# Kernel optimization log

Measured on AMD Instinct MI355X. Metric: run time of the kernel, lower is better.

Reference implementation:

```python
import jax, jax.numpy as jnp
import numpy as np

B, D, H, W = 8, 1024, 64, 64
NH = 16
HD = D // NH
EPS = 1e-5


def _pos_encoding(n, d, dtype):
    # standard 1D sinusoidal PE over flattened spatial positions, shape (n, d)
    pos = jnp.arange(n, dtype=jnp.float32)[:, None]
    i = jnp.arange(d)[None, :]
    rates = 1.0 / (10000.0 ** ((2 * (i // 2)).astype(jnp.float32) / d))
    ang = pos * rates
    pe = jnp.where(i % 2 == 0, jnp.sin(ang), jnp.cos(ang))
    return pe.astype(dtype)


def setup_inputs() -> dict:
    key = jax.random.key(0)
    ks = jax.random.split(key, 4)
    x = jax.random.normal(ks[0], (B, D, H, W), dtype=jnp.float32)
    context_token = jax.random.normal(ks[1], (B, 1, D), dtype=jnp.float32)
    Wqkv = jax.random.normal(ks[2], (3 * D, D), dtype=jnp.float32) * 0.02
    bqkv = jnp.zeros((3 * D,), dtype=jnp.float32)
    Wo = jax.random.normal(ks[3], (D, D), dtype=jnp.float32) * 0.02
    bo = jnp.zeros((D,), dtype=jnp.float32)
    gamma = jnp.ones((D,), dtype=jnp.float32)
    beta = jnp.zeros((D,), dtype=jnp.float32)
    return {"x": x, "context_token": context_token, "Wqkv": Wqkv, "bqkv": bqkv,
            "Wo": Wo, "bo": bo, "gamma": gamma, "beta": beta}


def reference(x, context_token, Wqkv, bqkv, Wo, bo, gamma, beta):
    b, d, h, w = x.shape
    hw = h * w
    # x_flat: (B, HW, D); add positional encoding
    x_flat = x.reshape(b, d, hw).transpose(0, 2, 1)
    x_flat = x_flat + _pos_encoding(hw, d, x.dtype)[None]
    xc = jnp.concatenate([context_token, x_flat], axis=1)  # (B, S, D), S = HW+1
    s = hw + 1

    qkv = xc @ Wqkv.T + bqkv                                 # (B, S, 3D)
    q, k, v = jnp.split(qkv, 3, axis=-1)
    k = k.reshape(b, s, NH, HD)
    v = v.reshape(b, s, NH, HD)
    scale = 1.0 / jnp.sqrt(jnp.asarray(HD, x.dtype))

    # Star attention: CLS query (row 0) attends to all keys
    q0 = q[:, 0].reshape(b, NH, HD)                          # (B, NH, HD)
    scores = jnp.einsum('bhd,bshd->bhs', q0, k) * scale      # (B, NH, S)
    probs = jax.nn.softmax(scores, axis=-1)
    cls_out = jnp.einsum('bhs,bshd->bhd', probs, v).reshape(b, d)

    # Token queries attend only to the CLS key -> softmax over 1 elem = 1 -> v_cls
    v_cls = v[:, 0].reshape(b, d)                            # (B, D)
    tok_out = jnp.broadcast_to(v_cls[:, None, :], (b, hw, d))

    attn = jnp.concatenate([cls_out[:, None, :], tok_out], axis=1)  # (B, S, D)
    attn = attn @ Wo.T + bo

    res = attn + xc
    mu = jnp.mean(res, axis=-1, keepdims=True)
    var = jnp.mean((res - mu) ** 2, axis=-1, keepdims=True)
    y = (res - mu) * jax.lax.rsqrt(var + EPS) * gamma + beta

    context_token_out = y[:, 0:1, :]
    feature_map_out = y[:, 1:, :].transpose(0, 2, 1).reshape(b, d, h, w)
    return feature_map_out, context_token_out
```

## Files before the change

kernel.cpp:

```cpp
#include <hip/hip_runtime.h>
#include <math.h>

#define B_ 8
#define D_ 1024
#define HW_ 4096
#define NH_ 16
#define EPS_ 1e-5f

#define PE_OFF   0u
#define UT_OFF   4194304u
#define TB_OFF   4325376u
#define SC_OFF   4333568u
#define Q0_OFF   4857856u
#define VCLS_OFF 4866048u
#define P0_OFF   4874240u
#define MU_OFF   4874368u
#define RS_OFF   4907136u
#define W_OFF    4939904u
#define CLS_OFF  5070976u
#define R0_OFF   5079168u

__global__ void k_pe(float* __restrict__ pe) {
    int idx = blockIdx.x * 256 + threadIdx.x;
    int p  = idx & (HW_ - 1);
    int dp = idx >> 12;
    float e = (float)(2 * dp);
    float rate = exp2f(e * (-13.287712379549449f / 1024.0f));
    float ang = (float)p * rate;
    float s, c;
    sincosf(ang, &s, &c);
    pe[(size_t)(2 * dp) * HW_ + p]     = s;
    pe[(size_t)(2 * dp + 1) * HW_ + p] = c;
}

__global__ void k_qv(const float* __restrict__ Wqkv, const float* __restrict__ bqkv,
                     const float* __restrict__ ctx,
                     float* __restrict__ q0, float* __restrict__ vcls) {
    int wid  = (blockIdx.x * 256 + threadIdx.x) >> 6;
    int lane = threadIdx.x & 63;
    int isv  = wid >> 13;
    int r    = wid & 8191;
    int b = r >> 10, i = r & 1023;
    int row = isv ? (2 * D_ + i) : i;
    const float4* wr = (const float4*)(Wqkv + (size_t)row * D_);
    const float4* cb = (const float4*)(ctx + b * D_);
    float acc = 0.0f;
    for (int k = lane; k < 256; k += 64) {
        float4 a = wr[k], c = cb[k];
        acc += a.x * c.x + a.y * c.y + a.z * c.z + a.w * c.w;
    }
    for (int o = 32; o; o >>= 1) acc += __shfl_down(acc, o);
    if (lane == 0) {
        float v = acc + bqkv[row];
        if (isv) vcls[b * D_ + i] = v; else q0[b * D_ + i] = v;
    }
}

__global__ void k_u_tb(const float* __restrict__ Wqkv,
                       const float* __restrict__ Wo, const float* __restrict__ bo,
                       const float* __restrict__ q0, const float* __restrict__ vcls,
                       float* __restrict__ u_t, float* __restrict__ t_b) {
    if (blockIdx.x < 128) {
        int b = blockIdx.x >> 4, h = blockIdx.x & 15;
        int t = threadIdx.x;
        float a0 = 0, a1 = 0, a2 = 0, a3 = 0;
        const float* q0h = q0 + b * D_ + h * 64;
        for (int j = 0; j < 64; ++j) {
            float qj = q0h[j];
            const float* wr = Wqkv + (size_t)(D_ + h * 64 + j) * D_;
            a0 += qj * wr[t];
            a1 += qj * wr[t + 256];
            a2 += qj * wr[t + 512];
            a3 += qj * wr[t + 768];
        }
        float* ub = u_t + (size_t)(b * D_) * NH_ + h;
        ub[(size_t)t * 16]          = 0.125f * a0;
        ub[(size_t)(t + 256) * 16]  = 0.125f * a1;
        ub[(size_t)(t + 512) * 16]  = 0.125f * a2;
        ub[(size_t)(t + 768) * 16]  = 0.125f * a3;
    } else {
        int wid  = (blockIdx.x - 128) * 4 + (threadIdx.x >> 6);
        int lane = threadIdx.x & 63;
        int b = wid >> 10, i = wid & 1023;
        const float4* wr = (const float4*)(Wo + (size_t)i * D_);
        const float4* vb = (const float4*)(vcls + b * D_);
        float acc = 0.0f;
        for (int k = lane; k < 256; k += 64) {
            float4 a = wr[k], c = vb[k];
            acc += a.x * c.x + a.y * c.y + a.z * c.z + a.w * c.w;
        }
        for (int o = 32; o; o >>= 1) acc += __shfl_down(acc, o);
        if (lane == 0) t_b[b * D_ + i] = acc + bo[i];
    }
}

__global__ __launch_bounds__(1024) void k_scores(
        const float* __restrict__ x, const float* __restrict__ pe,
        const float* __restrict__ u_t, const float* __restrict__ t_b,
        float* __restrict__ scores, float* __restrict__ mu_o, float* __restrict__ rs_o) {
    int tid = threadIdx.x;
    int wave = tid >> 6, lane = tid & 63;
    int b = blockIdx.y;
    int pbase = blockIdx.x * 128;
    int p0 = pbase + lane * 2;
    const float* xb  = x  + (size_t)b * D_ * HW_ + p0;
    const float* peb = pe + p0;
    const float* tb  = t_b + b * D_;
    float acc0[16], acc1[16];
    #pragma unroll
    for (int h = 0; h < 16; ++h) { acc0[h] = 0.f; acc1[h] = 0.f; }
    float s0 = 0.f, s1 = 0.f, q0s = 0.f, q1s = 0.f;
    int dbeg = wave * 64;
    #pragma unroll 2
    for (int i = 0; i < 64; ++i) {
        int d = dbeg + i;
        float2 xv = *(const float2*)(xb  + (size_t)d * HW_);
        float2 pv = *(const float2*)(peb + (size_t)d * HW_);
        float xc0 = xv.x + pv.x, xc1 = xv.y + pv.y;
        float tbd = tb[d];
        float r0 = xc0 + tbd, r1 = xc1 + tbd;
        s0 += r0; s1 += r1; q0s += r0 * r0; q1s += r1 * r1;
        const float* up = u_t + ((size_t)(b * D_ + d) << 4);
        #pragma unroll
        for (int h = 0; h < 16; ++h) {
            float u = up[h];
            acc0[h] += u * xc0;
            acc1[h] += u * xc1;
        }
    }
    __shared__ float red[16][4][128];
    #pragma unroll 1
    for (int c = 0; c < 4; ++c) {
        #pragma unroll
        for (int j = 0; j < 4; ++j) {
            red[wave][j][lane * 2]     = acc0[4 * c + j];
            red[wave][j][lane * 2 + 1] = acc1[4 * c + j];
        }
        __syncthreads();
        if (tid < 512) {
            int hh = tid >> 7, p = tid & 127;
            float s = 0.f;
            #pragma unroll
            for (int w2 = 0; w2 < 16; ++w2) s += red[w2][hh][p];
            scores[(size_t)(b * 16 + 4 * c + hh) * HW_ + pbase + p] = s;
        }
        __syncthreads();
    }
    red[wave][0][lane * 2]     = s0;
    red[wave][0][lane * 2 + 1] = s1;
    red[wave][1][lane * 2]     = q0s;
    red[wave][1][lane * 2 + 1] = q1s;
    __syncthreads();
    if (tid < 128) {
        float S = 0.f, Q = 0.f;
        #pragma unroll
        for (int w2 = 0; w2 < 16; ++w2) { S += red[w2][0][tid]; Q += red[w2][1][tid]; }
        float mu = S * (1.0f / 1024.0f);
        float var = Q * (1.0f / 1024.0f) - mu * mu;
        mu_o[b * HW_ + pbase + tid] = mu;
        rs_o[b * HW_ + pbase + tid] = rsqrtf(var + EPS_);
    }
}

__global__ void k_softmax(const float* __restrict__ scores, const float* __restrict__ u_t,
                          const float* __restrict__ ctx,
                          float* __restrict__ probs_tok, float* __restrict__ probs0) {
    int b = blockIdx.x >> 4, h = blockIdx.x & 15;
    int t = threadIdx.x;
    __shared__ float lds[256];
    float part = 0.0f;
    for (int d = t; d < D_; d += 256)
        part += u_t[(size_t)(b * D_ + d) * 16 + h] * ctx[b * D_ + d];
    lds[t] = part; __syncthreads();
    for (int o = 128; o; o >>= 1) { if (t < o) lds[t] += lds[t + o]; __syncthreads(); }
    float s0 = lds[0];
    __syncthreads();
    const float4* sr = (const float4*)(scores + (size_t)(b * 16 + h) * HW_);
    float4 v[4];
    float m = s0;
    #pragma unroll
    for (int k = 0; k < 4; ++k) {
        v[k] = sr[t + 256 * k];
        m = fmaxf(m, fmaxf(fmaxf(v[k].x, v[k].y), fmaxf(v[k].z, v[k].w)));
    }
    lds[t] = m; __syncthreads();
    for (int o = 128; o; o >>= 1) { if (t < o) lds[t] = fmaxf(lds[t], lds[t + o]); __syncthreads(); }
    m = lds[0];
    __syncthreads();
    float zs = 0.0f;
    #pragma unroll
    for (int k = 0; k < 4; ++k) {
        v[k].x = expf(v[k].x - m); v[k].y = expf(v[k].y - m);
        v[k].z = expf(v[k].z - m); v[k].w = expf(v[k].w - m);
        zs += v[k].x + v[k].y + v[k].z + v[k].w;
    }
    float e0 = expf(s0 - m);
    lds[t] = zs; __syncthreads();
    for (int o = 128; o; o >>= 1) { if (t < o) lds[t] += lds[t + o]; __syncthreads(); }
    float inv = 1.0f / (lds[0] + e0);
    float4* pr = (float4*)(probs_tok + (size_t)(b * 16 + h) * HW_);
    #pragma unroll
    for (int k = 0; k < 4; ++k) {
        float4 o4 = v[k];
        o4.x *= inv; o4.y *= inv; o4.z *= inv; o4.w *= inv;
        pr[t + 256 * k] = o4;
    }
    if (t == 0) probs0[b * 16 + h] = e0 * inv;
}

__global__ __launch_bounds__(256) void k_wacc2(
        const float* __restrict__ x, const float* __restrict__ pe,
        const float* __restrict__ probs, const float* __restrict__ p0v,
        const float* __restrict__ ctx, const float* __restrict__ t_b,
        const float* __restrict__ mu_i, const float* __restrict__ rs_i,
        const float* __restrict__ gamma, const float* __restrict__ beta,
        float* __restrict__ w, float* __restrict__ out) {
    int wave = threadIdx.x >> 6, lane = threadIdx.x & 63;
    int b = blockIdx.y;
    int d0 = (blockIdx.x * 4 + wave) * 4;
    const float* xb = x + (size_t)b * D_ * HW_;
    const float* pb = probs + (size_t)b * 16 * HW_;
    float* ob = out + (size_t)b * D_ * HW_;
    float tbv[4], gv[4], bev[4];
    #pragma unroll
    for (int r = 0; r < 4; ++r) {
        tbv[r] = t_b[b * D_ + d0 + r];
        gv[r]  = gamma[d0 + r];
        bev[r] = beta[d0 + r];
    }
    float acc[4][16];
    #pragma unroll
    for (int r = 0; r < 4; ++r)
        #pragma unroll
        for (int h = 0; h < 16; ++h) acc[r][h] = 0.f;
    #pragma unroll 1
    for (int it = 0; it < 16; ++it) {
        int p = it * 256 + lane * 4;
        float4 xc4[4];
        #pragma unroll
        for (int r = 0; r < 4; ++r) {
            float4 xv = *(const float4*)(xb + (size_t)(d0 + r) * HW_ + p);
            float4 pv = *(const float4*)(pe + (size_t)(d0 + r) * HW_ + p);
            xc4[r].x = xv.x + pv.x; xc4[r].y = xv.y + pv.y;
            xc4[r].z = xv.z + pv.z; xc4[r].w = xv.w + pv.w;
        }
        float4 m4 = *(const float4*)(mu_i + b * HW_ + p);
        float4 r4 = *(const float4*)(rs_i + b * HW_ + p);
        #pragma unroll
        for (int r = 0; r < 4; ++r) {
            float4 o4;
            o4.x = (xc4[r].x + tbv[r] - m4.x) * r4.x * gv[r] + bev[r];
            o4.y = (xc4[r].y + tbv[r] - m4.y) * r4.y * gv[r] + bev[r];
            o4.z = (xc4[r].z + tbv[r] - m4.z) * r4.z * gv[r] + bev[r];
            o4.w = (xc4[r].w + tbv[r] - m4.w) * r4.w * gv[r] + bev[r];
            *(float4*)(ob + (size_t)(d0 + r) * HW_ + p) = o4;
        }
        #pragma unroll
        for (int h = 0; h < 16; ++h) {
            float4 pr = *(const float4*)(pb + (size_t)h * HW_ + p);
            #pragma unroll
            for (int r = 0; r < 4; ++r)
                acc[r][h] += pr.x * xc4[r].x + pr.y * xc4[r].y +
                             pr.z * xc4[r].z + pr.w * xc4[r].w;
        }
    }
    #pragma unroll
    for (int r = 0; r < 4; ++r)
        #pragma unroll
        for (int h = 0; h < 16; ++h) {
            float v = acc[r][h];
            for (int o = 32; o; o >>= 1) v += __shfl_down(v, o);
            acc[r][h] = v;
        }
    if (lane == 0) {
        #pragma unroll
        for (int h = 0; h < 16; ++h) {
            float pp = p0v[b * 16 + h];
            #pragma unroll
            for (int r = 0; r < 4; ++r)
                w[(size_t)(b * 16 + h) * D_ + d0 + r] = acc[r][h] + pp * ctx[b * D_ + d0 + r];
        }
    }
}

__global__ void k_cls(const float* __restrict__ Wqkv, const float* __restrict__ bqkv,
                      const float* __restrict__ w, float* __restrict__ cls) {
    int wid  = (blockIdx.x * 256 + threadIdx.x) >> 6;
    int lane = threadIdx.x & 63;
    int b = wid >> 10, i = wid & 1023, h = i >> 6;
    const float4* wr = (const float4*)(Wqkv + (size_t)(2 * D_ + i) * D_);
    const float4* wb = (const float4*)(w + (size_t)(b * 16 + h) * D_);
    float acc = 0.0f;
    for (int k = lane; k < 256; k += 64) {
        float4 a = wr[k], c = wb[k];
        acc += a.x * c.x + a.y * c.y + a.z * c.z + a.w * c.w;
    }
    for (int o = 32; o; o >>= 1) acc += __shfl_down(acc, o);
    if (lane == 0) cls[b * D_ + i] = acc + bqkv[2 * D_ + i];
}

__global__ void k_attn0(const float* __restrict__ Wo, const float* __restrict__ bo,
                        const float* __restrict__ cls, const float* __restrict__ ctx,
                        float* __restrict__ res0) {
    int wid  = (blockIdx.x * 256 + threadIdx.x) >> 6;
    int lane = threadIdx.x & 63;
    int b = wid >> 10, i = wid & 1023;
    const float4* wr = (const float4*)(Wo + (size_t)i * D_);
    const float4* cb = (const float4*)(cls + b * D_);
    float acc = 0.0f;
    for (int k = lane; k < 256; k += 64) {
        float4 a = wr[k], c = cb[k];
        acc += a.x * c.x + a.y * c.y + a.z * c.z + a.w * c.w;
    }
    for (int o = 32; o; o >>= 1) acc += __shfl_down(acc, o);
    if (lane == 0) res0[b * D_ + i] = acc + bo[i] + ctx[b * D_ + i];
}

__global__ void k_ln0(const float* __restrict__ res0, const float* __restrict__ gamma,
                      const float* __restrict__ beta, float* __restrict__ out) {
    int b = blockIdx.x, t = threadIdx.x;
    __shared__ float lds[512];
    float v[4];
    float s = 0.0f, sq = 0.0f;
    #pragma unroll
    for (int k = 0; k < 4; ++k) {
        v[k] = res0[b * D_ + t + 256 * k];
        s += v[k]; sq += v[k] * v[k];
    }
    lds[t] = s; lds[256 + t] = sq; __syncthreads();
    for (int o = 128; o; o >>= 1) {
        if (t < o) { lds[t] += lds[t + o]; lds[256 + t] += lds[256 + t + o]; }
        __syncthreads();
    }
    float mu = lds[0] * (1.0f / D_);
    float var = lds[256] * (1.0f / D_) - mu * mu;
    float rstd = rsqrtf(var + EPS_);
    #pragma unroll
    for (int k = 0; k < 4; ++k) {
        int i = t + 256 * k;
        out[(size_t)B_ * D_ * HW_ + b * D_ + i] = (v[k] - mu) * rstd * gamma[i] + beta[i];
    }
}

extern "C" void kernel_launch(void* const* d_in, const int* in_sizes, int n_in,
                              void* d_out, int out_size, void* d_ws, size_t ws_size,
                              hipStream_t stream) {
    const float* x     = (const float*)d_in[0];
    const float* ctx   = (const float*)d_in[1];
    const float* Wqkv  = (const float*)d_in[2];
    const float* bqkv  = (const float*)d_in[3];
    const float* Wo    = (const float*)d_in[4];
    const float* bo    = (const float*)d_in[5];
    const float* gamma = (const float*)d_in[6];
    const float* beta  = (const float*)d_in[7];
    float* out = (float*)d_out;
    float* ws  = (float*)d_ws;

    float* pe   = ws + PE_OFF;
    float* u_t  = ws + UT_OFF;
    float* t_b  = ws + TB_OFF;
    float* sc   = ws + SC_OFF;
    float* q0   = ws + Q0_OFF;
    float* vcls = ws + VCLS_OFF;
    float* p0   = ws + P0_OFF;
    float* mu   = ws + MU_OFF;
    float* rs   = ws + RS_OFF;
    float* w    = ws + W_OFF;
    float* cls  = ws + CLS_OFF;
    float* r0   = ws + R0_OFF;

    k_pe<<<dim3(8192), dim3(256), 0, stream>>>(pe);
    k_qv<<<dim3(4096), dim3(256), 0, stream>>>(Wqkv, bqkv, ctx, q0, vcls);
    k_u_tb<<<dim3(2176), dim3(256), 0, stream>>>(Wqkv, Wo, bo, q0, vcls, u_t, t_b);
    k_scores<<<dim3(32, 8), dim3(1024), 0, stream>>>(x, pe, u_t, t_b, sc, mu, rs);
    k_softmax<<<dim3(128), dim3(256), 0, stream>>>(sc, u_t, ctx, sc, p0);
    k_wacc2<<<dim3(64, 8), dim3(256), 0, stream>>>(x, pe, sc, p0, ctx, t_b, mu, rs,
                                                   gamma, beta, w, out);
    k_cls<<<dim3(2048), dim3(256), 0, stream>>>(Wqkv, bqkv, w, cls);
    k_attn0<<<dim3(2048), dim3(256), 0, stream>>>(Wo, bo, cls, ctx, r0);
    k_ln0<<<dim3(8), dim3(256), 0, stream>>>(r0, gamma, beta, out);
}
```

Measured before the change: 429.0 us.

## Split scores over D and weighted accumulation over positions into partial buffers

The scores kernel now splits the 1024-wide D reduction into 8 slices. Each slice writes partial scores and partial sum and sum-of-squares to workspace. A new stats kernel and the softmax kernel sum those partials. The weighted-accumulation kernel splits positions into 4 chunks, writing partial w vectors that the cls kernel sums. The aim is many more, smaller blocks (float4 loads, 256 threads) so the GPU fills better than with one 1024-thread block per CU, at the cost of extra partial-buffer traffic and one more launch.

```diff
diff --git a/kernel.cpp b/kernel.cpp
--- a/kernel.cpp
+++ b/kernel.cpp
@@ -10,15 +10,17 @@
 #define PE_OFF   0u
 #define UT_OFF   4194304u
 #define TB_OFF   4325376u
-#define SC_OFF   4333568u
-#define Q0_OFF   4857856u
-#define VCLS_OFF 4866048u
-#define P0_OFF   4874240u
-#define MU_OFF   4874368u
-#define RS_OFF   4907136u
-#define W_OFF    4939904u
-#define CLS_OFF  5070976u
-#define R0_OFF   5079168u
+#define SCP_OFF  4333568u
+#define SP_OFF   8527872u
+#define QP_OFF   8790016u
+#define WP_OFF   8527872u
+#define Q0_OFF   9052160u
+#define VCLS_OFF 9060352u
+#define P0_OFF   9068544u
+#define MU_OFF   9068672u
+#define RS_OFF   9101440u
+#define CLS_OFF  9134208u
+#define R0_OFF   9142400u
 
 __global__ void k_pe(float* __restrict__ pe) {
     int idx = blockIdx.x * 256 + threadIdx.x;
@@ -94,77 +96,83 @@
     }
 }
 
-__global__ __launch_bounds__(1024) void k_scores(
+#define FMA4(A, U) { (A).x += (U) * xc.x; (A).y += (U) * xc.y; \
+                     (A).z += (U) * xc.z; (A).w += (U) * xc.w; }
+
+__global__ __launch_bounds__(256, 4) void k_scores2(
         const float* __restrict__ x, const float* __restrict__ pe,
         const float* __restrict__ u_t, const float* __restrict__ t_b,
-        float* __restrict__ scores, float* __restrict__ mu_o, float* __restrict__ rs_o) {
+        float* __restrict__ scp, float* __restrict__ sp, float* __restrict__ qp) {
     int tid = threadIdx.x;
     int wave = tid >> 6, lane = tid & 63;
     int b = blockIdx.y;
-    int pbase = blockIdx.x * 128;
-    int p0 = pbase + lane * 2;
+    int ptile = (blockIdx.x & 15) * 256;
+    int ds = blockIdx.x >> 4;
+    int p0 = ptile + lane * 4;
+    int dbeg = ds * 128 + wave * 32;
     const float* xb  = x  + (size_t)b * D_ * HW_ + p0;
     const float* peb = pe + p0;
     const float* tb  = t_b + b * D_;
-    float acc0[16], acc1[16];
-    #pragma unroll
-    for (int h = 0; h < 16; ++h) { acc0[h] = 0.f; acc1[h] = 0.f; }
-    float s0 = 0.f, s1 = 0.f, q0s = 0.f, q1s = 0.f;
-    int dbeg = wave * 64;
-    #pragma unroll 2
-    for (int i = 0; i < 64; ++i) {
+    float4 acc[16];
+    #pragma unroll
+    for (int h = 0; h < 16; ++h) acc[h] = make_float4(0.f, 0.f, 0.f, 0.f);
+    float4 s4 = make_float4(0.f, 0.f, 0.f, 0.f);
+    float4 q4 = make_float4(0.f, 0.f, 0.f, 0.f);
+    #pragma unroll 4
+    for (int i = 0; i < 32; ++i) {
         int d = dbeg + i;
-        float2 xv = *(const float2*)(xb  + (size_t)d * HW_);
-        float2 pv = *(const float2*)(peb + (size_t)d * HW_);
-        float xc0 = xv.x + pv.x, xc1 = xv.y + pv.y;
+        float4 xv = *(const float4*)(xb  + (size_t)d * HW_);
+        float4 pv = *(const float4*)(peb + (size_t)d * HW_);
+        float4 xc = make_float4(xv.x + pv.x, xv.y + pv.y, xv.z + pv.z, xv.w + pv.w);
         float tbd = tb[d];
-        float r0 = xc0 + tbd, r1 = xc1 + tbd;
-        s0 += r0; s1 += r1; q0s += r0 * r0; q1s += r1 * r1;
-        const float* up = u_t + ((size_t)(b * D_ + d) << 4);
-        #pragma unroll
-        for (int h = 0; h < 16; ++h) {
-            float u = up[h];
-            acc0[h] += u * xc0;
-            acc1[h] += u * xc1;
-        }
-    }
-    __shared__ float red[16][4][128];
+        float4 r = make_float4(xc.x + tbd, xc.y + tbd, xc.z + tbd, xc.w + tbd);
+        s4.x += r.x; s4.y += r.y; s4.z += r.z; s4.w += r.w;
+        q4.x += r.x * r.x; q4.y += r.y * r.y; q4.z += r.z * r.z; q4.w += r.w * r.w;
+        const float4* up = (const float4*)(u_t + ((size_t)(b * D_ + d) << 4));
+        float4 u0 = up[0], u1 = up[1], u2 = up[2], u3 = up[3];
+        FMA4(acc[0],  u0.x) FMA4(acc[1],  u0.y) FMA4(acc[2],  u0.z) FMA4(acc[3],  u0.w)
+        FMA4(acc[4],  u1.x) FMA4(acc[5],  u1.y) FMA4(acc[6],  u1.z) FMA4(acc[7],  u1.w)
+        FMA4(acc[8],  u2.x) FMA4(acc[9],  u2.y) FMA4(acc[10], u2.z) FMA4(acc[11], u2.w)
+        FMA4(acc[12], u3.x) FMA4(acc[13], u3.y) FMA4(acc[14], u3.z) FMA4(acc[15], u3.w)
+    }
+    __shared__ float red[4][4][256];
     #pragma unroll 1
     for (int c = 0; c < 4; ++c) {
+        if (c) __syncthreads();
+        #pragma unroll
+        for (int j = 0; j < 4; ++j)
+            *(float4*)&red[wave][j][lane * 4] = acc[c * 4 + j];
+        __syncthreads();
         #pragma unroll
         for (int j = 0; j < 4; ++j) {
-            red[wave][j][lane * 2]     = acc0[4 * c + j];
-            red[wave][j][lane * 2 + 1] = acc1[4 * c + j];
-        }
-        __syncthreads();
-        if (tid < 512) {
-            int hh = tid >> 7, p = tid & 127;
-            float s = 0.f;
-            #pragma unroll
-            for (int w2 = 0; w2 < 16; ++w2) s += red[w2][hh][p];
-            scores[(size_t)(b * 16 + 4 * c + hh) * HW_ + pbase + p] = s;
-        }
-        __syncthreads();
-    }
-    red[wave][0][lane * 2]     = s0;
-    red[wave][0][lane * 2 + 1] = s1;
-    red[wave][1][lane * 2]     = q0s;
-    red[wave][1][lane * 2 + 1] = q1s;
+            float s = red[0][j][tid] + red[1][j][tid] + red[2][j][tid] + red[3][j][tid];
+            scp[(size_t)ds * 524288 + (size_t)(b * 16 + c * 4 + j) * HW_ + ptile + tid] = s;
+        }
+    }
     __syncthreads();
-    if (tid < 128) {
-        float S = 0.f, Q = 0.f;
-        #pragma unroll
-        for (int w2 = 0; w2 < 16; ++w2) { S += red[w2][0][tid]; Q += red[w2][1][tid]; }
-        float mu = S * (1.0f / 1024.0f);
-        float var = Q * (1.0f / 1024.0f) - mu * mu;
-        mu_o[b * HW_ + pbase + tid] = mu;
-        rs_o[b * HW_ + pbase + tid] = rsqrtf(var + EPS_);
-    }
-}
-
-__global__ void k_softmax(const float* __restrict__ scores, const float* __restrict__ u_t,
-                          const float* __restrict__ ctx,
-                          float* __restrict__ probs_tok, float* __restrict__ probs0) {
+    *(float4*)&red[wave][0][lane * 4] = s4;
+    *(float4*)&red[wave][1][lane * 4] = q4;
+    __syncthreads();
+    float S = red[0][0][tid] + red[1][0][tid] + red[2][0][tid] + red[3][0][tid];
+    float Q = red[0][1][tid] + red[1][1][tid] + red[2][1][tid] + red[3][1][tid];
+    sp[ds * 32768 + b * HW_ + ptile + tid] = S;
+    qp[ds * 32768 + b * HW_ + ptile + tid] = Q;
+}
+
+__global__ void k_stats(const float* __restrict__ sp, const float* __restrict__ qp,
+                        float* __restrict__ mu_o, float* __restrict__ rs_o) {
+    int i = blockIdx.x * 256 + threadIdx.x;
+    float S = 0.f, Q = 0.f;
+    #pragma unroll
+    for (int ds = 0; ds < 8; ++ds) { S += sp[ds * 32768 + i]; Q += qp[ds * 32768 + i]; }
+    float mu = S * (1.0f / 1024.0f);
+    float var = Q * (1.0f / 1024.0f) - mu * mu;
+    mu_o[i] = mu;
+    rs_o[i] = rsqrtf(var + EPS_);
+}
+
+__global__ void k_softmax2(float* __restrict__ scp, const float* __restrict__ u_t,
+                           const float* __restrict__ ctx, float* __restrict__ probs0) {
     int b = blockIdx.x >> 4, h = blockIdx.x & 15;
     int t = threadIdx.x;
     __shared__ float lds[256];
@@ -175,13 +183,19 @@
     for (int o = 128; o; o >>= 1) { if (t < o) lds[t] += lds[t + o]; __syncthreads(); }
     float s0 = lds[0];
     __syncthreads();
-    const float4* sr = (const float4*)(scores + (size_t)(b * 16 + h) * HW_);
+    size_t row = (size_t)(b * 16 + h) * HW_;
     float4 v[4];
     float m = s0;
     #pragma unroll
     for (int k = 0; k < 4; ++k) {
-        v[k] = sr[t + 256 * k];
-        m = fmaxf(m, fmaxf(fmaxf(v[k].x, v[k].y), fmaxf(v[k].z, v[k].w)));
+        float4 vk = make_float4(0.f, 0.f, 0.f, 0.f);
+        #pragma unroll
+        for (int ds = 0; ds < 8; ++ds) {
+            float4 pvk = ((const float4*)(scp + (size_t)ds * 524288 + row))[t + 256 * k];
+            vk.x += pvk.x; vk.y += pvk.y; vk.z += pvk.z; vk.w += pvk.w;
+        }
+        v[k] = vk;
+        m = fmaxf(m, fmaxf(fmaxf(vk.x, vk.y), fmaxf(vk.z, vk.w)));
     }
     lds[t] = m; __syncthreads();
     for (int o = 128; o; o >>= 1) { if (t < o) lds[t] = fmaxf(lds[t], lds[t + o]); __syncthreads(); }
@@ -198,7 +212,7 @@
     lds[t] = zs; __syncthreads();
     for (int o = 128; o; o >>= 1) { if (t < o) lds[t] += lds[t + o]; __syncthreads(); }
     float inv = 1.0f / (lds[0] + e0);
-    float4* pr = (float4*)(probs_tok + (size_t)(b * 16 + h) * HW_);
+    float4* pr = (float4*)(scp + row);
     #pragma unroll
     for (int k = 0; k < 4; ++k) {
         float4 o4 = v[k];
@@ -208,16 +222,18 @@
     if (t == 0) probs0[b * 16 + h] = e0 * inv;
 }
 
-__global__ __launch_bounds__(256) void k_wacc2(
+__global__ __launch_bounds__(256, 4) void k_wacc3(
         const float* __restrict__ x, const float* __restrict__ pe,
         const float* __restrict__ probs, const float* __restrict__ p0v,
         const float* __restrict__ ctx, const float* __restrict__ t_b,
         const float* __restrict__ mu_i, const float* __restrict__ rs_i,
         const float* __restrict__ gamma, const float* __restrict__ beta,
-        float* __restrict__ w, float* __restrict__ out) {
+        float* __restrict__ wp, float* __restrict__ out) {
     int wave = threadIdx.x >> 6, lane = threadIdx.x & 63;
     int b = blockIdx.y;
-    int d0 = (blockIdx.x * 4 + wave) * 4;
+    int dgrp = blockIdx.x >> 2, pc = blockIdx.x & 3;
+    int d0 = (dgrp * 4 + wave) * 4;
+    int pbase = pc * 1024;
     const float* xb = x + (size_t)b * D_ * HW_;
     const float* pb = probs + (size_t)b * 16 * HW_;
     float* ob = out + (size_t)b * D_ * HW_;
@@ -234,8 +250,8 @@
         #pragma unroll
         for (int h = 0; h < 16; ++h) acc[r][h] = 0.f;
     #pragma unroll 1
-    for (int it = 0; it < 16; ++it) {
-        int p = it * 256 + lane * 4;
+    for (int it = 0; it < 4; ++it) {
+        int p = pbase + it * 256 + lane * 4;
         float4 xc4[4];
         #pragma unroll
         for (int r = 0; r < 4; ++r) {
@@ -275,25 +291,31 @@
     if (lane == 0) {
         #pragma unroll
         for (int h = 0; h < 16; ++h) {
-            float pp = p0v[b * 16 + h];
+            float extra = (pc == 0) ? p0v[b * 16 + h] : 0.f;
             #pragma unroll
             for (int r = 0; r < 4; ++r)
-                w[(size_t)(b * 16 + h) * D_ + d0 + r] = acc[r][h] + pp * ctx[b * D_ + d0 + r];
-        }
-    }
-}
-
-__global__ void k_cls(const float* __restrict__ Wqkv, const float* __restrict__ bqkv,
-                      const float* __restrict__ w, float* __restrict__ cls) {
+                wp[(size_t)pc * 131072 + (size_t)(b * 16 + h) * D_ + d0 + r] =
+                    acc[r][h] + extra * ctx[b * D_ + d0 + r];
+        }
+    }
+}
+
+__global__ void k_cls2(const float* __restrict__ Wqkv, const float* __restrict__ bqkv,
+                       const float* __restrict__ wp, float* __restrict__ cls) {
     int wid  = (blockIdx.x * 256 + threadIdx.x) >> 6;
     int lane = threadIdx.x & 63;
     int b = wid >> 10, i = wid & 1023, h = i >> 6;
     const float4* wr = (const float4*)(Wqkv + (size_t)(2 * D_ + i) * D_);
-    const float4* wb = (const float4*)(w + (size_t)(b * 16 + h) * D_);
+    const float4* w0 = (const float4*)(wp + (size_t)(b * 16 + h) * D_);
     float acc = 0.0f;
     for (int k = lane; k < 256; k += 64) {
-        float4 a = wr[k], c = wb[k];
-        acc += a.x * c.x + a.y * c.y + a.z * c.z + a.w * c.w;
+        float4 a = wr[k];
+        float4 c0 = w0[k], c1 = w0[k + 32768], c2 = w0[k + 65536], c3 = w0[k + 98304];
+        float cx = c0.x + c1.x + c2.x + c3.x;
+        float cy = c0.y + c1.y + c2.y + c3.y;
+        float cz = c0.z + c1.z + c2.z + c3.z;
+        float cw = c0.w + c1.w + c2.w + c3.w;
+        acc += a.x * cx + a.y * cy + a.z * cz + a.w * cw;
     }
     for (int o = 32; o; o >>= 1) acc += __shfl_down(acc, o);
     if (lane == 0) cls[b * D_ + i] = acc + bqkv[2 * D_ + i];
@@ -359,24 +381,27 @@
     float* pe   = ws + PE_OFF;
     float* u_t  = ws + UT_OFF;
     float* t_b  = ws + TB_OFF;
-    float* sc   = ws + SC_OFF;
+    float* scp  = ws + SCP_OFF;
+    float* sp   = ws + SP_OFF;
+    float* qp   = ws + QP_OFF;
+    float* wpb  = ws + WP_OFF;
     float* q0   = ws + Q0_OFF;
     float* vcls = ws + VCLS_OFF;
     float* p0   = ws + P0_OFF;
     float* mu   = ws + MU_OFF;
     float* rs   = ws + RS_OFF;
-    float* w    = ws + W_OFF;
     float* cls  = ws + CLS_OFF;
     float* r0   = ws + R0_OFF;
 
     k_pe<<<dim3(8192), dim3(256), 0, stream>>>(pe);
     k_qv<<<dim3(4096), dim3(256), 0, stream>>>(Wqkv, bqkv, ctx, q0, vcls);
     k_u_tb<<<dim3(2176), dim3(256), 0, stream>>>(Wqkv, Wo, bo, q0, vcls, u_t, t_b);
-    k_scores<<<dim3(32, 8), dim3(1024), 0, stream>>>(x, pe, u_t, t_b, sc, mu, rs);
-    k_softmax<<<dim3(128), dim3(256), 0, stream>>>(sc, u_t, ctx, sc, p0);
-    k_wacc2<<<dim3(64, 8), dim3(256), 0, stream>>>(x, pe, sc, p0, ctx, t_b, mu, rs,
-                                                   gamma, beta, w, out);
-    k_cls<<<dim3(2048), dim3(256), 0, stream>>>(Wqkv, bqkv, w, cls);
+    k_scores2<<<dim3(128, 8), dim3(256), 0, stream>>>(x, pe, u_t, t_b, scp, sp, qp);
+    k_softmax2<<<dim3(128), dim3(256), 0, stream>>>(scp, u_t, ctx, p0);
+    k_stats<<<dim3(128), dim3(256), 0, stream>>>(sp, qp, mu, rs);
+    k_wacc3<<<dim3(256, 8), dim3(256), 0, stream>>>(x, pe, scp, p0, ctx, t_b, mu, rs,
+                                                    gamma, beta, wpb, out);
+    k_cls2<<<dim3(2048), dim3(256), 0, stream>>>(Wqkv, bqkv, wpb, cls);
     k_attn0<<<dim3(2048), dim3(256), 0, stream>>>(Wo, bo, cls, ctx, r0);
     k_ln0<<<dim3(8), dim3(256), 0, stream>>>(r0, gamma, beta, out);
 }
```

Result: slower. 727.7 us (+69.6%).

## Compute positional encoding inline and split score reduction over D for parallelism

Applied to the files above, without the earlier changes.

Drops the precomputed positional-encoding buffer and recomputes sin/cos on the fly with hardware sin/cos intrinsics, removing a large 16 MB write plus two re-reads of it. The scores kernel is split across 8 D-slices (2048 blocks of 256 threads instead of 256 blocks of 1024) with u_t staged in LDS. It writes partial scores and partial stats, which a new stats kernel and the softmax then reduce. Probabilities are stored transposed (position-major, 16 heads contiguous) and the weighted-accumulate kernel uses one d row per wave for more blocks. The cost is extra partial-sum traffic, an extra launch, and possible precision loss from the approximate hardware sin/cos on large angles.

```diff
diff --git a/kernel.cpp b/kernel.cpp
--- a/kernel.cpp
+++ b/kernel.cpp
@@ -7,31 +7,23 @@
 #define NH_ 16
 #define EPS_ 1e-5f
 
-#define PE_OFF   0u
-#define UT_OFF   4194304u
-#define TB_OFF   4325376u
-#define SC_OFF   4333568u
-#define Q0_OFF   4857856u
-#define VCLS_OFF 4866048u
-#define P0_OFF   4874240u
-#define MU_OFF   4874368u
-#define RS_OFF   4907136u
-#define W_OFF    4939904u
-#define CLS_OFF  5070976u
-#define R0_OFF   5079168u
-
-__global__ void k_pe(float* __restrict__ pe) {
-    int idx = blockIdx.x * 256 + threadIdx.x;
-    int p  = idx & (HW_ - 1);
-    int dp = idx >> 12;
-    float e = (float)(2 * dp);
-    float rate = exp2f(e * (-13.287712379549449f / 1024.0f));
-    float ang = (float)p * rate;
-    float s, c;
-    sincosf(ang, &s, &c);
-    pe[(size_t)(2 * dp) * HW_ + p]     = s;
-    pe[(size_t)(2 * dp + 1) * HW_ + p] = c;
-}
+#define RATE_C (-13.287712379549449f / 512.0f)
+#define INV2PI 0.15915494309189535f
+
+#define UT_OFF   0u
+#define TB_OFF   131072u
+#define SCP_OFF  139264u
+#define SP_OFF   4333568u
+#define QP_OFF   4595712u
+#define PT_OFF   4857856u
+#define W_OFF    5382144u
+#define Q0_OFF   5513216u
+#define VCLS_OFF 5521408u
+#define P0_OFF   5529600u
+#define MU_OFF   5529728u
+#define RS_OFF   5562496u
+#define CLS_OFF  5595264u
+#define R0_OFF   5603456u
 
 __global__ void k_qv(const float* __restrict__ Wqkv, const float* __restrict__ bqkv,
                      const float* __restrict__ ctx,
@@ -94,77 +86,121 @@
     }
 }
 
-__global__ __launch_bounds__(1024) void k_scores(
-        const float* __restrict__ x, const float* __restrict__ pe,
-        const float* __restrict__ u_t, const float* __restrict__ t_b,
-        float* __restrict__ scores, float* __restrict__ mu_o, float* __restrict__ rs_o) {
+__global__ __launch_bounds__(256) void k_scoresA(
+        const float* __restrict__ x, const float* __restrict__ u_t,
+        const float* __restrict__ t_b,
+        float* __restrict__ scp, float* __restrict__ sp, float* __restrict__ qp) {
     int tid = threadIdx.x;
     int wave = tid >> 6, lane = tid & 63;
     int b = blockIdx.y;
-    int pbase = blockIdx.x * 128;
-    int p0 = pbase + lane * 2;
-    const float* xb  = x  + (size_t)b * D_ * HW_ + p0;
-    const float* peb = pe + p0;
-    const float* tb  = t_b + b * D_;
-    float acc0[16], acc1[16];
-    #pragma unroll
-    for (int h = 0; h < 16; ++h) { acc0[h] = 0.f; acc1[h] = 0.f; }
-    float s0 = 0.f, s1 = 0.f, q0s = 0.f, q1s = 0.f;
-    int dbeg = wave * 64;
+    int ptile = (blockIdx.x & 31) * 128;
+    int ds = blockIdx.x >> 5;
+    int p0 = ptile + lane * 2;
+
+    __shared__ float uts[128 * 16];
+    __shared__ float tbs[128];
+    __shared__ float rrev[64];
+    __shared__ float red[4][4][128];
+    {
+        const float4* src = (const float4*)(u_t + ((size_t)(b * D_ + ds * 128) << 4));
+        float4* dst = (float4*)uts;
+        dst[tid]       = src[tid];
+        dst[tid + 256] = src[tid + 256];
+        if (tid < 128) tbs[tid] = t_b[b * D_ + ds * 128 + tid];
+        if (tid < 64)  rrev[tid] = exp2f((float)(ds * 64 + tid) * RATE_C) * INV2PI;
+    }
+    __syncthreads();
+
+    float accA[16], accB[16];
+    #pragma unroll
+    for (int h = 0; h < 16; ++h) { accA[h] = 0.f; accB[h] = 0.f; }
+    float sA = 0.f, sB = 0.f, qA = 0.f, qB = 0.f;
+    const float* xb = x + (size_t)b * D_ * HW_ + (size_t)(ds * 128 + wave * 32) * HW_ + p0;
+    float fp0 = (float)p0, fp1 = fp0 + 1.0f;
+
     #pragma unroll 2
-    for (int i = 0; i < 64; ++i) {
-        int d = dbeg + i;
-        float2 xv = *(const float2*)(xb  + (size_t)d * HW_);
-        float2 pv = *(const float2*)(peb + (size_t)d * HW_);
-        float xc0 = xv.x + pv.x, xc1 = xv.y + pv.y;
-        float tbd = tb[d];
-        float r0 = xc0 + tbd, r1 = xc1 + tbd;
-        s0 += r0; s1 += r1; q0s += r0 * r0; q1s += r1 * r1;
-        const float* up = u_t + ((size_t)(b * D_ + d) << 4);
-        #pragma unroll
-        for (int h = 0; h < 16; ++h) {
-            float u = up[h];
-            acc0[h] += u * xc0;
-            acc1[h] += u * xc1;
-        }
-    }
-    __shared__ float red[16][4][128];
+    for (int i = 0; i < 16; ++i) {
+        int dloc = wave * 32 + i * 2;
+        float2 xe = *(const float2*)(xb + (size_t)(i * 2) * HW_);
+        float2 xo = *(const float2*)(xb + (size_t)(i * 2 + 1) * HW_);
+        float rr = rrev[wave * 16 + i];
+        float rv0 = fp0 * rr, rv1 = fp1 * rr;
+        rv0 -= floorf(rv0); rv1 -= floorf(rv1);
+        float sn0 = __builtin_amdgcn_sinf(rv0), cs0 = __builtin_amdgcn_cosf(rv0);
+        float sn1 = __builtin_amdgcn_sinf(rv1), cs1 = __builtin_amdgcn_cosf(rv1);
+        float xAe = xe.x + sn0, xBe = xe.y + sn1;
+        float xAo = xo.x + cs0, xBo = xo.y + cs1;
+        float te = tbs[dloc], to = tbs[dloc + 1];
+        float rAe = xAe + te, rBe = xBe + te, rAo = xAo + to, rBo = xBo + to;
+        sA += rAe + rAo; sB += rBe + rBo;
+        qA += rAe * rAe + rAo * rAo; qB += rBe * rBe + rBo * rBo;
+        const float4* u4 = (const float4*)(uts + dloc * 16);
+        float4 e0 = u4[0], e1 = u4[1], o0 = u4[4], o1 = u4[5];
+        accA[0] += e0.x * xAe + o0.x * xAo;  accB[0] += e0.x * xBe + o0.x * xBo;
+        accA[1] += e0.y * xAe + o0.y * xAo;  accB[1] += e0.y * xBe + o0.y * xBo;
+        accA[2] += e0.z * xAe + o0.z * xAo;  accB[2] += e0.z * xBe + o0.z * xBo;
+        accA[3] += e0.w * xAe + o0.w * xAo;  accB[3] += e0.w * xBe + o0.w * xBo;
+        accA[4] += e1.x * xAe + o1.x * xAo;  accB[4] += e1.x * xBe + o1.x * xBo;
+        accA[5] += e1.y * xAe + o1.y * xAo;  accB[5] += e1.y * xBe + o1.y * xBo;
+        accA[6] += e1.z * xAe + o1.z * xAo;  accB[6] += e1.z * xBe + o1.z * xBo;
+        accA[7] += e1.w * xAe + o1.w * xAo;  accB[7] += e1.w * xBe + o1.w * xBo;
+        float4 e2 = u4[2], e3 = u4[3], o2 = u4[6], o3 = u4[7];
+        accA[8]  += e2.x * xAe + o2.x * xAo;  accB[8]  += e2.x * xBe + o2.x * xBo;
+        accA[9]  += e2.y * xAe + o2.y * xAo;  accB[9]  += e2.y * xBe + o2.y * xBo;
+        accA[10] += e2.z * xAe + o2.z * xAo;  accB[10] += e2.z * xBe + o2.z * xBo;
+        accA[11] += e2.w * xAe + o2.w * xAo;  accB[11] += e2.w * xBe + o2.w * xBo;
+        accA[12] += e3.x * xAe + o3.x * xAo;  accB[12] += e3.x * xBe + o3.x * xBo;
+        accA[13] += e3.y * xAe + o3.y * xAo;  accB[13] += e3.y * xBe + o3.y * xBo;
+        accA[14] += e3.z * xAe + o3.z * xAo;  accB[14] += e3.z * xBe + o3.z * xBo;
+        accA[15] += e3.w * xAe + o3.w * xAo;  accB[15] += e3.w * xBe + o3.w * xBo;
+    }
+
     #pragma unroll 1
     for (int c = 0; c < 4; ++c) {
+        if (c) __syncthreads();
         #pragma unroll
         for (int j = 0; j < 4; ++j) {
-            red[wave][j][lane * 2]     = acc0[4 * c + j];
-            red[wave][j][lane * 2 + 1] = acc1[4 * c + j];
+            red[wave][j][lane * 2]     = accA[c * 4 + j];
+            red[wave][j][lane * 2 + 1] = accB[c * 4 + j];
         }
         __syncthreads();
-        if (tid < 512) {
-            int hh = tid >> 7, p = tid & 127;
-            float s = 0.f;
-            #pragma unroll
-            for (int w2 = 0; w2 < 16; ++w2) s += red[w2][hh][p];
-            scores[(size_t)(b * 16 + 4 * c + hh) * HW_ + pbase + p] = s;
-        }
-        __syncthreads();
-    }
-    red[wave][0][lane * 2]     = s0;
-    red[wave][0][lane * 2 + 1] = s1;
-    red[wave][1][lane * 2]     = q0s;
-    red[wave][1][lane * 2 + 1] = q1s;
+        int j = tid >> 7, p = tid & 127;
+        #pragma unroll
+        for (int jj = 0; jj < 2; ++jj) {
+            int jr = j + jj * 2;
+            float s = red[0][jr][p] + red[1][jr][p] + red[2][jr][p] + red[3][jr][p];
+            scp[(size_t)ds * 524288 + (size_t)(b * 16 + c * 4 + jr) * HW_ + ptile + p] = s;
+        }
+    }
+    __syncthreads();
+    red[wave][0][lane * 2]     = sA;
+    red[wave][0][lane * 2 + 1] = sB;
+    red[wave][1][lane * 2]     = qA;
+    red[wave][1][lane * 2 + 1] = qB;
     __syncthreads();
     if (tid < 128) {
-        float S = 0.f, Q = 0.f;
-        #pragma unroll
-        for (int w2 = 0; w2 < 16; ++w2) { S += red[w2][0][tid]; Q += red[w2][1][tid]; }
-        float mu = S * (1.0f / 1024.0f);
-        float var = Q * (1.0f / 1024.0f) - mu * mu;
-        mu_o[b * HW_ + pbase + tid] = mu;
-        rs_o[b * HW_ + pbase + tid] = rsqrtf(var + EPS_);
-    }
-}
-
-__global__ void k_softmax(const float* __restrict__ scores, const float* __restrict__ u_t,
-                          const float* __restrict__ ctx,
-                          float* __restrict__ probs_tok, float* __restrict__ probs0) {
+        float S = red[0][0][tid] + red[1][0][tid] + red[2][0][tid] + red[3][0][tid];
+        float Q = red[0][1][tid] + red[1][1][tid] + red[2][1][tid] + red[3][1][tid];
+        sp[ds * 32768 + b * HW_ + ptile + tid] = S;
+        qp[ds * 32768 + b * HW_ + ptile + tid] = Q;
+    }
+}
+
+__global__ void k_stats(const float* __restrict__ sp, const float* __restrict__ qp,
+                        float* __restrict__ mu_o, float* __restrict__ rs_o) {
+    int i = blockIdx.x * 256 + threadIdx.x;
+    float S = 0.f, Q = 0.f;
+    #pragma unroll
+    for (int ds = 0; ds < 8; ++ds) { S += sp[ds * 32768 + i]; Q += qp[ds * 32768 + i]; }
+    float mu = S * (1.0f / 1024.0f);
+    float var = Q * (1.0f / 1024.0f) - mu * mu;
+    mu_o[i] = mu;
+    rs_o[i] = rsqrtf(var + EPS_);
+}
+
+__global__ void k_softmaxT(const float* __restrict__ scp, const float* __restrict__ u_t,
+                           const float* __restrict__ ctx,
+                           float* __restrict__ pt, float* __restrict__ probs0) {
     int b = blockIdx.x >> 4, h = blockIdx.x & 15;
     int t = threadIdx.x;
     __shared__ float lds[256];
@@ -175,13 +211,19 @@
     for (int o = 128; o; o >>= 1) { if (t < o) lds[t] += lds[t + o]; __syncthreads(); }
     float s0 = lds[0];
     __syncthreads();
-    const float4* sr = (const float4*)(scores + (size_t)(b * 16 + h) * HW_);
+    size_t row = (size_t)(b * 16 + h) * HW_;
     float4 v[4];
     float m = s0;
     #pragma unroll
     for (int k = 0; k < 4; ++k) {
-        v[k] = sr[t + 256 * k];
-        m = fmaxf(m, fmaxf(fmaxf(v[k].x, v[k].y), fmaxf(v[k].z, v[k].w)));
+        float4 vk = make_float4(0.f, 0.f, 0.f, 0.f);
+        #pragma unroll
+        for (int ds = 0; ds < 8; ++ds) {
+            float4 pvk = ((const float4*)(scp + (size_t)ds * 524288 + row))[t + 256 * k];
+            vk.x += pvk.x; vk.y += pvk.y; vk.z += pvk.z; vk.w += pvk.w;
+        }
+        v[k] = vk;
+        m = fmaxf(m, fmaxf(fmaxf(vk.x, vk.y), fmaxf(vk.z, vk.w)));
     }
     lds[t] = m; __syncthreads();
     for (int o = 128; o; o >>= 1) { if (t < o) lds[t] = fmaxf(lds[t], lds[t + o]); __syncthreads(); }
@@ -198,88 +240,87 @@
     lds[t] = zs; __syncthreads();
     for (int o = 128; o; o >>= 1) { if (t < o) lds[t] += lds[t + o]; __syncthreads(); }
     float inv = 1.0f / (lds[0] + e0);
-    float4* pr = (float4*)(probs_tok + (size_t)(b * 16 + h) * HW_);
+    float* ptb = pt + (size_t)b * HW_ * 16 + h;
     #pragma unroll
     for (int k = 0; k < 4; ++k) {
-        float4 o4 = v[k];
-        o4.x *= inv; o4.y *= inv; o4.z *= inv; o4.w *= inv;
-        pr[t + 256 * k] = o4;
+        int p = 4 * (t + 256 * k);
+        ptb[(size_t)(p + 0) * 16] = v[k].x * inv;
+        ptb[(size_t)(p + 1) * 16] = v[k].y * inv;
+        ptb[(size_t)(p + 2) * 16] = v[k].z * inv;
+        ptb[(size_t)(p + 3) * 16] = v[k].w * inv;
     }
     if (t == 0) probs0[b * 16 + h] = e0 * inv;
 }
 
-__global__ __launch_bounds__(256) void k_wacc2(
-        const float* __restrict__ x, const float* __restrict__ pe,
-        const float* __restrict__ probs, const float* __restrict__ p0v,
-        const float* __restrict__ ctx, const float* __restrict__ t_b,
-        const float* __restrict__ mu_i, const float* __restrict__ rs_i,
-        const float* __restrict__ gamma, const float* __restrict__ beta,
+__global__ __launch_bounds__(256) void k_waccB(
+        const float* __restrict__ x, const float* __restrict__ pt,
+        const float* __restrict__ p0v, const float* __restrict__ ctx,
+        const float* __restrict__ t_b, const float* __restrict__ mu_i,
+        const float* __restrict__ rs_i, const float* __restrict__ gamma,
+        const float* __restrict__ beta,
         float* __restrict__ w, float* __restrict__ out) {
     int wave = threadIdx.x >> 6, lane = threadIdx.x & 63;
     int b = blockIdx.y;
-    int d0 = (blockIdx.x * 4 + wave) * 4;
-    const float* xb = x + (size_t)b * D_ * HW_;
-    const float* pb = probs + (size_t)b * 16 * HW_;
-    float* ob = out + (size_t)b * D_ * HW_;
-    float tbv[4], gv[4], bev[4];
-    #pragma unroll
-    for (int r = 0; r < 4; ++r) {
-        tbv[r] = t_b[b * D_ + d0 + r];
-        gv[r]  = gamma[d0 + r];
-        bev[r] = beta[d0 + r];
-    }
-    float acc[4][16];
-    #pragma unroll
-    for (int r = 0; r < 4; ++r)
-        #pragma unroll
-        for (int h = 0; h < 16; ++h) acc[r][h] = 0.f;
+    int d = blockIdx.x * 4 + wave;
+    float tb = t_b[b * D_ + d], g = gamma[d], be = beta[d];
+    int odd = d & 1;
+    float rr = exp2f((float)(d >> 1) * RATE_C) * INV2PI;
+    const float* xr  = x + (size_t)b * D_ * HW_ + (size_t)d * HW_;
+    const float* ptb = pt + (size_t)b * HW_ * 16;
+    const float* mub = mu_i + b * HW_;
+    const float* rsb = rs_i + b * HW_;
+    float* or_ = out + (size_t)b * D_ * HW_ + (size_t)d * HW_;
+    float acc[16];
+    #pragma unroll
+    for (int h = 0; h < 16; ++h) acc[h] = 0.f;
+
     #pragma unroll 1
     for (int it = 0; it < 16; ++it) {
         int p = it * 256 + lane * 4;
-        float4 xc4[4];
+        float4 xv = *(const float4*)(xr + p);
+        float4 m4 = *(const float4*)(mub + p);
+        float4 r4 = *(const float4*)(rsb + p);
+        float rv0 = (float)p * rr;
+        float rv1 = rv0 + rr, rv2 = rv1 + rr, rv3 = rv2 + rr;
+        rv0 -= floorf(rv0); rv1 -= floorf(rv1); rv2 -= floorf(rv2); rv3 -= floorf(rv3);
+        float pe0 = odd ? __builtin_amdgcn_cosf(rv0) : __builtin_amdgcn_sinf(rv0);
+        float pe1 = odd ? __builtin_amdgcn_cosf(rv1) : __builtin_amdgcn_sinf(rv1);
+        float pe2 = odd ? __builtin_amdgcn_cosf(rv2) : __builtin_amdgcn_sinf(rv2);
+        float pe3 = odd ? __builtin_amdgcn_cosf(rv3) : __builtin_amdgcn_sinf(rv3);
+        float xc0 = xv.x + pe0, xc1 = xv.y + pe1, xc2 = xv.z + pe2, xc3 = xv.w + pe3;
+        float4 o4;
+        o4.x = (xc0 + tb - m4.x) * r4.x * g + be;
+        o4.y = (xc1 + tb - m4.y) * r4.y * g + be;
+        o4.z = (xc2 + tb - m4.z) * r4.z * g + be;
+        o4.w = (xc3 + tb - m4.w) * r4.w * g + be;
+        *(float4*)(or_ + p) = o4;
+        const float4* q4 = (const float4*)(ptb + (size_t)p * 16);
         #pragma unroll
-        for (int r = 0; r < 4; ++r) {
-            float4 xv = *(const float4*)(xb + (size_t)(d0 + r) * HW_ + p);
-            float4 pv = *(const float4*)(pe + (size_t)(d0 + r) * HW_ + p);
-            xc4[r].x = xv.x + pv.x; xc4[r].y = xv.y + pv.y;
-            xc4[r].z = xv.z + pv.z; xc4[r].w = xv.w + pv.w;
-        }
-        float4 m4 = *(const float4*)(mu_i + b * HW_ + p);
-        float4 r4 = *(const float4*)(rs_i + b * HW_ + p);
+        for (int j = 0; j < 4; ++j) {
+            float xcj = (j == 0) ? xc0 : (j == 1) ? xc1 : (j == 2) ? xc2 : xc3;
+            float4 a0 = q4[j * 4 + 0], a1 = q4[j * 4 + 1];
+            float4 a2 = q4[j * 4 + 2], a3 = q4[j * 4 + 3];
+            acc[0]  += a0.x * xcj; acc[1]  += a0.y * xcj;
+            acc[2]  += a0.z * xcj; acc[3]  += a0.w * xcj;
+            acc[4]  += a1.x * xcj; acc[5]  += a1.y * xcj;
+            acc[6]  += a1.z * xcj; acc[7]  += a1.w * xcj;
+            acc[8]  += a2.x * xcj; acc[9]  += a2.y * xcj;
+            acc[10] += a2.z * xcj; acc[11] += a2.w * xcj;
+            acc[12] += a3.x * xcj; acc[13] += a3.y * xcj;
+            acc[14] += a3.z * xcj; acc[15] += a3.w * xcj;
+        }
+    }
+    #pragma unroll
+    for (int h = 0; h < 16; ++h) {
+        float v = acc[h];
+        for (int o = 32; o; o >>= 1) v += __shfl_down(v, o);
+        acc[h] = v;
+    }
+    if (lane == 0) {
+        float cx = ctx[b * D_ + d];
         #pragma unroll
-        for (int r = 0; r < 4; ++r) {
-            float4 o4;
-            o4.x = (xc4[r].x + tbv[r] - m4.x) * r4.x * gv[r] + bev[r];
-            o4.y = (xc4[r].y + tbv[r] - m4.y) * r4.y * gv[r] + bev[r];
-            o4.z = (xc4[r].z + tbv[r] - m4.z) * r4.z * gv[r] + bev[r];
-            o4.w = (xc4[r].w + tbv[r] - m4.w) * r4.w * gv[r] + bev[r];
-            *(float4*)(ob + (size_t)(d0 + r) * HW_ + p) = o4;
-        }
-        #pragma unroll
-        for (int h = 0; h < 16; ++h) {
-            float4 pr = *(const float4*)(pb + (size_t)h * HW_ + p);
-            #pragma unroll
-            for (int r = 0; r < 4; ++r)
-                acc[r][h] += pr.x * xc4[r].x + pr.y * xc4[r].y +
-                             pr.z * xc4[r].z + pr.w * xc4[r].w;
-        }
-    }
-    #pragma unroll
-    for (int r = 0; r < 4; ++r)
-        #pragma unroll
-        for (int h = 0; h < 16; ++h) {
-            float v = acc[r][h];
-            for (int o = 32; o; o >>= 1) v += __shfl_down(v, o);
-            acc[r][h] = v;
-        }
-    if (lane == 0) {
-        #pragma unroll
-        for (int h = 0; h < 16; ++h) {
-            float pp = p0v[b * 16 + h];
-            #pragma unroll
-            for (int r = 0; r < 4; ++r)
-                w[(size_t)(b * 16 + h) * D_ + d0 + r] = acc[r][h] + pp * ctx[b * D_ + d0 + r];
-        }
+        for (int h = 0; h < 16; ++h)
+            w[(size_t)(b * 16 + h) * D_ + d] = acc[h] + p0v[b * 16 + h] * cx;
     }
 }
 
@@ -356,26 +397,28 @@
     float* out = (float*)d_out;
     float* ws  = (float*)d_ws;
 
-    float* pe   = ws + PE_OFF;
     float* u_t  = ws + UT_OFF;
     float* t_b  = ws + TB_OFF;
-    float* sc   = ws + SC_OFF;
+    float* scp  = ws + SCP_OFF;
+    float* sp   = ws + SP_OFF;
+    float* qp   = ws + QP_OFF;
+    float* pt   = ws + PT_OFF;
+    float* w    = ws + W_OFF;
     float* q0   = ws + Q0_OFF;
     float* vcls = ws + VCLS_OFF;
     float* p0   = ws + P0_OFF;
     float* mu   = ws + MU_OFF;
     float* rs   = ws + RS_OFF;
-    float* w    = ws + W_OFF;
     float* cls  = ws + CLS_OFF;
     float* r0   = ws + R0_OFF;
 
-    k_pe<<<dim3(8192), dim3(256), 0, stream>>>(pe);
     k_qv<<<dim3(4096), dim3(256), 0, stream>>>(Wqkv, bqkv, ctx, q0, vcls);
     k_u_tb<<<dim3(2176), dim3(256), 0, stream>>>(Wqkv, Wo, bo, q0, vcls, u_t, t_b);
-    k_scores<<<dim3(32, 8), dim3(1024), 0, stream>>>(x, pe, u_t, t_b, sc, mu, rs);
-    k_softmax<<<dim3(128), dim3(256), 0, stream>>>(sc, u_t, ctx, sc, p0);
-    k_wacc2<<<dim3(64, 8), dim3(256), 0, stream>>>(x, pe, sc, p0, ctx, t_b, mu, rs,
-                                                   gamma, beta, w, out);
+    k_scoresA<<<dim3(256, 8), dim3(256), 0, stream>>>(x, u_t, t_b, scp, sp, qp);
+    k_stats<<<dim3(128), dim3(256), 0, stream>>>(sp, qp, mu, rs);
+    k_softmaxT<<<dim3(128), dim3(256), 0, stream>>>(scp, u_t, ctx, pt, p0);
+    k_waccB<<<dim3(256, 8), dim3(256), 0, stream>>>(x, pt, p0, ctx, t_b, mu, rs,
+                                                    gamma, beta, w, out);
     k_cls<<<dim3(2048), dim3(256), 0, stream>>>(Wqkv, bqkv, w, cls);
     k_attn0<<<dim3(2048), dim3(256), 0, stream>>>(Wo, bo, cls, ctx, r0);
     k_ln0<<<dim3(8), dim3(256), 0, stream>>>(r0, gamma, beta, out);
```

After: 609.7 us. 42.1% more time.
